# Optimization experiments

Hardware: AMD Instinct MI355X
Metric: run time of the kernel (lower is better)

## Reference

```python
import jax, jax.numpy as jnp
import numpy as np

N, K, D = 65536, 1024, 512
ALPHA = 1.0

def setup_inputs() -> dict:
    key = jax.random.key(0)
    k1, k2 = jax.random.split(key)
    batch = jax.random.normal(k1, (N, D), dtype=jnp.float32)
    # Xavier uniform init for cluster centers: bound = sqrt(6/(K+D))
    bound = float(np.sqrt(6.0 / (K + D)))
    cluster_centers = jax.random.uniform(k2, (K, D), dtype=jnp.float32, minval=-bound, maxval=bound)
    return {"batch": batch, "cluster_centers": cluster_centers}

def reference(batch, cluster_centers):
    x_sq = jnp.sum(batch * batch, axis=1, keepdims=True)            # [N,1]
    c_sq = jnp.sum(cluster_centers * cluster_centers, axis=1)       # [K]
    cross = batch @ cluster_centers.T                               # [N,K]
    norm_squared = jnp.maximum(x_sq - 2.0 * cross + c_sq[None, :], 0.0)
    numerator = 1.0 / (1.0 + norm_squared / ALPHA)
    power = (ALPHA + 1.0) / 2.0
    numerator = numerator ** power
    return numerator / jnp.sum(numerator, axis=1, keepdims=True)
```

## Files before the change

### kernel.cpp

```cpp
#include <hip/hip_runtime.h>
#include <hip/hip_bf16.h>
#include <stdint.h>


#define N_ROWS 65536
#define K_CL   1024
#define D_DIM  512
#define BM     64
#define BK     64

typedef __attribute__((ext_vector_type(8))) short short8;
typedef __attribute__((ext_vector_type(4))) float f32x4;

__device__ __forceinline__ ushort f2bf(float f) {
    union { float f; uint32_t u; } v; v.f = f;
    uint32_t u = v.u;
    u += 0x7fffu + ((u >> 16) & 1u);
    return (ushort)(u >> 16);
}

__device__ __forceinline__ float waveReduceSum(float s) {
#pragma unroll
    for (int off = 32; off; off >>= 1) s += __shfl_down(s, off, 64);
    return s;
}

__global__ void prep_rows(const float* __restrict__ X, ushort* __restrict__ Xbf,
                          float* __restrict__ sq) {
    const int row  = blockIdx.x * 4 + (threadIdx.x >> 6);
    const int lane = threadIdx.x & 63;
    const float4* src = (const float4*)(X + (size_t)row * D_DIM);
    float4 a = src[lane * 2];
    float4 b = src[lane * 2 + 1];
    float s = (a.x*a.x + a.y*a.y) + (a.z*a.z + a.w*a.w)
            + (b.x*b.x + b.y*b.y) + (b.z*b.z + b.w*b.w);
    uint4 o;
    o.x = (uint32_t)f2bf(a.x) | ((uint32_t)f2bf(a.y) << 16);
    o.y = (uint32_t)f2bf(a.z) | ((uint32_t)f2bf(a.w) << 16);
    o.z = (uint32_t)f2bf(b.x) | ((uint32_t)f2bf(b.y) << 16);
    o.w = (uint32_t)f2bf(b.z) | ((uint32_t)f2bf(b.w) << 16);
    *(uint4*)(Xbf + (size_t)row * D_DIM + lane * 8) = o;
    s = waveReduceSum(s);
    if (lane == 0) sq[row] = s;
}

__global__ __launch_bounds__(512, 2) void gemm_fused(
    const ushort* __restrict__ A, const ushort* __restrict__ B,
    const float* __restrict__ xsq, const float* __restrict__ csq,
    float* __restrict__ out)
{
    __shared__ __align__(16) ushort smA[BM * BK];
    __shared__ __align__(16) ushort smB[K_CL * BK];

    const int tid  = threadIdx.x;
    const int w    = tid >> 6;
    const int lane = tid & 63;
    const int l4 = lane >> 4, l16 = lane & 15;
    const int rbase = blockIdx.x * BM;

    const int srow  = tid >> 3;
    const int sslot = (tid & 7) ^ (srow & 7);
    const ushort* gA = A + (size_t)(rbase + srow) * D_DIM + sslot * 8;
    const ushort* gB = B + (size_t)srow * D_DIM + sslot * 8;
    ushort* ldsA = smA + w * 512;

    f32x4 acc[4][8] = {};
    const int sw = (l16 & 7) << 4;

    for (int kt = 0; kt < D_DIM; kt += BK) {
        __builtin_amdgcn_global_load_lds(
            (const __attribute__((address_space(1))) void*)(gA + kt),
            (__attribute__((address_space(3))) void*)ldsA, 16, 0, 0);
#pragma unroll
        for (int c = 0; c < 16; ++c) {
            const ushort* src = gB + (size_t)c * 64 * D_DIM + kt;
            __builtin_amdgcn_global_load_lds(
                (const __attribute__((address_space(1))) void*)src,
                (__attribute__((address_space(3))) void*)(smB + c * 4096 + w * 512),
                16, 0, 0);
        }
        __syncthreads();

#pragma unroll
        for (int kk = 0; kk < 2; ++kk) {
            const int cb = kk * 64;
            short8 af[4], bf[8];
#pragma unroll
            for (int m = 0; m < 4; ++m) {
                const int row = m * 16 + l16;
                af[m] = *(const short8*)((const char*)smA
                        + row * 128 + ((cb + l4 * 16) ^ sw));
            }
#pragma unroll
            for (int n = 0; n < 8; ++n) {
                const int row = w * 128 + n * 16 + l16;
                bf[n] = *(const short8*)((const char*)smB
                        + row * 128 + ((cb + l4 * 16) ^ sw));
            }
#pragma unroll
            for (int m = 0; m < 4; ++m)
#pragma unroll
                for (int n = 0; n < 8; ++n)
                    acc[m][n] = __builtin_amdgcn_mfma_f32_16x16x32_bf16(
                        af[m], bf[n], acc[m][n], 0, 0, 0);
        }
        __syncthreads();
    }

    float xs[4][4];
#pragma unroll
    for (int m = 0; m < 4; ++m)
#pragma unroll
        for (int r = 0; r < 4; ++r)
            xs[m][r] = xsq[rbase + m * 16 + l4 * 4 + r];

    float s[4][4] = {{0.f}};
#pragma unroll
    for (int n = 0; n < 8; ++n) {
        const float cs = csq[w * 128 + n * 16 + l16];
#pragma unroll
        for (int m = 0; m < 4; ++m)
#pragma unroll
            for (int r = 0; r < 4; ++r) {
                float ns = fmaxf(xs[m][r] - 2.0f * acc[m][n][r] + cs, 0.0f);
                float p = 1.0f / (1.0f + ns);
                acc[m][n][r] = p;
                s[m][r] += p;
            }
    }
#pragma unroll
    for (int m = 0; m < 4; ++m)
#pragma unroll
        for (int r = 0; r < 4; ++r) {
            float v = s[m][r];
            v += __shfl_xor(v, 1, 64);
            v += __shfl_xor(v, 2, 64);
            v += __shfl_xor(v, 4, 64);
            v += __shfl_xor(v, 8, 64);
            s[m][r] = v;
        }
    float* smRS  = (float*)smA;
    float* smInv = (float*)smA + 512;
    if (l16 == 0) {
#pragma unroll
        for (int m = 0; m < 4; ++m)
#pragma unroll
            for (int r = 0; r < 4; ++r)
                smRS[w * 64 + m * 16 + l4 * 4 + r] = s[m][r];
    }
    __syncthreads();
    if (tid < 64) {
        float t = 0.f;
#pragma unroll
        for (int j = 0; j < 8; ++j) t += smRS[j * 64 + tid];
        smInv[tid] = 1.0f / t;
    }
    __syncthreads();

    float inv[4][4];
#pragma unroll
    for (int m = 0; m < 4; ++m)
#pragma unroll
        for (int r = 0; r < 4; ++r)
            inv[m][r] = smInv[m * 16 + l4 * 4 + r];

#pragma unroll
    for (int m = 0; m < 4; ++m)
#pragma unroll
        for (int n = 0; n < 8; ++n) {
            const int col = w * 128 + n * 16 + l16;
#pragma unroll
            for (int r = 0; r < 4; ++r) {
                const int row = rbase + m * 16 + l4 * 4 + r;
                out[(size_t)row * K_CL + col] = acc[m][n][r] * inv[m][r];
            }
        }
}

extern "C" void kernel_launch(void* const* d_in, const int* in_sizes, int n_in,
                              void* d_out, int out_size, void* d_ws, size_t ws_size,
                              hipStream_t stream) {
    const float* batch   = (const float*)d_in[0];
    const float* centers = (const float*)d_in[1];
    float* out = (float*)d_out;

    char* ws = (char*)d_ws;
    ushort* Abf = (ushort*)ws;
    ushort* Bbf = (ushort*)(ws + (size_t)N_ROWS * D_DIM * 2);
    float*  xsq = (float*)(ws + (size_t)N_ROWS * D_DIM * 2
                              + (size_t)K_CL * D_DIM * 2);
    float*  csq = xsq + N_ROWS;
    (void)in_sizes; (void)n_in; (void)out_size; (void)ws_size;

    prep_rows<<<K_CL / 4,   256, 0, stream>>>(centers, Bbf, csq);
    prep_rows<<<N_ROWS / 4, 256, 0, stream>>>(batch, Abf, xsq);
    gemm_fused<<<N_ROWS / BM, 512, 0, stream>>>(Abf, Bbf, xsq, csq, out);
}
```

Measured before the change: 207.2 us.

## Load B fragments directly from global and double-buffer A tile in LDS

Replaces the LDS staging of the full centers tile with per-wave direct global loads of B fragments into registers. Double-buffers the small A tile in LDS with prefetch of the next K slice, halving barrier count, and raises MFMA wave priority. This cuts LDS usage and sync overhead, which could raise occupancy. The risk is higher global/L2 load latency that is exposed without a register pipeline.

New measurement: 253.0 us. 1.22x slower.

```diff
diff --git a/kernel.cpp b/kernel.cpp
--- a/kernel.cpp
+++ b/kernel.cpp
@@ -7,7 +7,6 @@
 #define K_CL   1024
 #define D_DIM  512
 #define BM     64
-#define BK     64
 
 typedef __attribute__((ext_vector_type(8))) short short8;
 typedef __attribute__((ext_vector_type(4))) float f32x4;
@@ -49,8 +48,7 @@
     const float* __restrict__ xsq, const float* __restrict__ csq,
     float* __restrict__ out)
 {
-    __shared__ __align__(16) ushort smA[BM * BK];
-    __shared__ __align__(16) ushort smB[K_CL * BK];
+    __shared__ __align__(16) ushort smA[2][BM * 64];
 
     const int tid  = threadIdx.x;
     const int w    = tid >> 6;
@@ -61,50 +59,55 @@
     const int srow  = tid >> 3;
     const int sslot = (tid & 7) ^ (srow & 7);
     const ushort* gA = A + (size_t)(rbase + srow) * D_DIM + sslot * 8;
-    const ushort* gB = B + (size_t)srow * D_DIM + sslot * 8;
-    ushort* ldsA = smA + w * 512;
+    ushort* ldsA[2] = { &smA[0][0] + w * 512, &smA[1][0] + w * 512 };
+
+    const ushort* gB[8];
+#pragma unroll
+    for (int n = 0; n < 8; ++n)
+        gB[n] = B + (size_t)(w * 128 + n * 16 + l16) * D_DIM + l4 * 8;
 
     f32x4 acc[4][8] = {};
-    const int sw = (l16 & 7) << 4;
-
-    for (int kt = 0; kt < D_DIM; kt += BK) {
-        __builtin_amdgcn_global_load_lds(
-            (const __attribute__((address_space(1))) void*)(gA + kt),
-            (__attribute__((address_space(3))) void*)ldsA, 16, 0, 0);
-#pragma unroll
-        for (int c = 0; c < 16; ++c) {
-            const ushort* src = gB + (size_t)c * 64 * D_DIM + kt;
+    const int swz = (l16 & 7) << 4;
+
+    __builtin_amdgcn_global_load_lds(
+        (const __attribute__((address_space(1))) void*)gA,
+        (__attribute__((address_space(3))) void*)ldsA[0], 16, 0, 0);
+    __syncthreads();
+
+#pragma unroll
+    for (int s = 0; s < 16; ++s) {
+        const int kt  = s * 32;
+        const int buf = (s >> 1) & 1;
+
+        short8 bf[8];
+#pragma unroll
+        for (int n = 0; n < 8; ++n)
+            bf[n] = *(const short8*)(gB[n] + kt);
+
+        if ((s & 1) == 0 && s < 14)
             __builtin_amdgcn_global_load_lds(
-                (const __attribute__((address_space(1))) void*)src,
-                (__attribute__((address_space(3))) void*)(smB + c * 4096 + w * 512),
-                16, 0, 0);
+                (const __attribute__((address_space(1))) void*)(gA + kt + 64),
+                (__attribute__((address_space(3))) void*)ldsA[buf ^ 1], 16, 0, 0);
+
+        short8 af[4];
+        const int cb = (s & 1) * 64;
+#pragma unroll
+        for (int m = 0; m < 4; ++m) {
+            const int row = m * 16 + l16;
+            af[m] = *(const short8*)((const char*)&smA[buf][0]
+                    + row * 128 + ((cb + l4 * 16) ^ swz));
         }
-        __syncthreads();
-
-#pragma unroll
-        for (int kk = 0; kk < 2; ++kk) {
-            const int cb = kk * 64;
-            short8 af[4], bf[8];
-#pragma unroll
-            for (int m = 0; m < 4; ++m) {
-                const int row = m * 16 + l16;
-                af[m] = *(const short8*)((const char*)smA
-                        + row * 128 + ((cb + l4 * 16) ^ sw));
-            }
-#pragma unroll
-            for (int n = 0; n < 8; ++n) {
-                const int row = w * 128 + n * 16 + l16;
-                bf[n] = *(const short8*)((const char*)smB
-                        + row * 128 + ((cb + l4 * 16) ^ sw));
-            }
-#pragma unroll
-            for (int m = 0; m < 4; ++m)
-#pragma unroll
-                for (int n = 0; n < 8; ++n)
-                    acc[m][n] = __builtin_amdgcn_mfma_f32_16x16x32_bf16(
-                        af[m], bf[n], acc[m][n], 0, 0, 0);
-        }
-        __syncthreads();
+
+        __builtin_amdgcn_s_setprio(1);
+#pragma unroll
+        for (int m = 0; m < 4; ++m)
+#pragma unroll
+            for (int n = 0; n < 8; ++n)
+                acc[m][n] = __builtin_amdgcn_mfma_f32_16x16x32_bf16(
+                    af[m], bf[n], acc[m][n], 0, 0, 0);
+        __builtin_amdgcn_s_setprio(0);
+
+        if (s & 1) __syncthreads();
     }
 
     float xs[4][4];
@@ -139,8 +142,8 @@
             v += __shfl_xor(v, 8, 64);
             s[m][r] = v;
         }
-    float* smRS  = (float*)smA;
-    float* smInv = (float*)smA + 512;
+    float* smRS  = (float*)&smA[0][0];
+    float* smInv = (float*)&smA[0][0] + 512;
     if (l16 == 0) {
 #pragma unroll
         for (int m = 0; m < 4; ++m)
```
